# Performance work log

Measured on AMD Instinct MI355X. Metric: run time of the kernel, lower is better.

Reference implementation:

```python
import jax, jax.numpy as jnp
import numpy as np

H = 56; W = 56; WS = 7; SS = 3; HEADS = 12; DIM = 384

def _rel_pos_index(ws):
    coords = np.stack(np.meshgrid(np.arange(ws), np.arange(ws), indexing='ij'))  # (2, ws, ws)
    cf = coords.reshape(2, -1)
    rel = (cf[:, :, None] - cf[:, None, :]).transpose(1, 2, 0).astype(np.int64)  # (N, N, 2)
    rel[:, :, 0] += ws - 1
    rel[:, :, 1] += ws - 1
    rel[:, :, 0] *= 2 * ws - 1
    return jnp.asarray(rel.sum(-1))  # (N, N)

def _attn_mask(h, w, ws, ss):
    img = np.zeros((h, w))
    cnt = 0
    for hs in (slice(0, -ws), slice(-ws, -ss), slice(-ss, None)):
        for wsl in (slice(0, -ws), slice(-ws, -ss), slice(-ss, None)):
            img[hs, wsl] = cnt
            cnt += 1
    mw = img.reshape(h // ws, ws, w // ws, ws).transpose(0, 2, 1, 3).reshape(-1, ws * ws)
    am = mw[:, None, :] - mw[:, :, None]
    return jnp.asarray(np.where(am != 0, -100.0, 0.0).astype(np.float32))  # (nW, N, N)

REL_IDX = _rel_pos_index(WS)
ATTN_MASK = _attn_mask(H, W, WS, SS)

def _ln(x, g, b):
    mu = x.mean(-1, keepdims=True)
    var = x.var(-1, keepdims=True)  # biased, matches torch LayerNorm
    return (x - mu) / jnp.sqrt(var + 1e-5) * g + b

def setup_inputs():
    key = jax.random.key(0)
    ks = jax.random.split(key, 8)
    C = DIM
    Hd = 4 * C
    s = lambda k, shp: jax.random.normal(k, shp, jnp.float32) * 0.02
    return dict(
        x=jax.random.normal(ks[0], (32, H * W, C), jnp.float32),
        norm1_g=jnp.ones((C,), jnp.float32), norm1_b=jnp.zeros((C,), jnp.float32),
        qkv_w=s(ks[1], (3 * C, C)), qkv_b=jnp.zeros((3 * C,), jnp.float32),
        rpb_table=s(ks[2], ((2 * WS - 1) ** 2, HEADS)),
        proj_w=s(ks[3], (C, C)), proj_b=jnp.zeros((C,), jnp.float32),
        norm2_g=jnp.ones((C,), jnp.float32), norm2_b=jnp.zeros((C,), jnp.float32),
        fc1_w=s(ks[4], (Hd, C)), fc1_b=jnp.zeros((Hd,), jnp.float32),
        fc2_w=s(ks[5], (C, Hd)), fc2_b=jnp.zeros((C,), jnp.float32),
    )

def reference(x, norm1_g, norm1_b, qkv_w, qkv_b, rpb_table, proj_w, proj_b,
              norm2_g, norm2_b, fc1_w, fc1_b, fc2_w, fc2_b):
    B, L, C = x.shape
    h = HEADS
    d = C // h
    N = WS * WS
    nW = (H // WS) * (W // WS)
    shortcut = x
    y = _ln(x, norm1_g, norm1_b).reshape(B, H, W, C)
    # cyclic shift
    y = jnp.roll(y, (-SS, -SS), axis=(1, 2))
    # window partition -> (B*nW, N, C)
    y = y.reshape(B, H // WS, WS, W // WS, WS, C).transpose(0, 1, 3, 2, 4, 5).reshape(B * nW, N, C)
    # windowed attention
    qkv = (y @ qkv_w.T + qkv_b).reshape(B * nW, N, 3, h, d).transpose(2, 0, 3, 1, 4)
    q, k, v = qkv[0], qkv[1], qkv[2]  # (B*nW, h, N, d)
    scale = d ** -0.5
    attn = jnp.einsum('whnd,whmd->whnm', q * scale, k)
    bias = rpb_table[REL_IDX.reshape(-1)].reshape(N, N, h).transpose(2, 0, 1)  # (h, N, N)
    attn = attn + bias[None]
    attn = attn.reshape(B, nW, h, N, N) + ATTN_MASK[None, :, None]
    attn = jax.nn.softmax(attn.reshape(B * nW, h, N, N), axis=-1)
    out = jnp.einsum('whnm,whmd->whnd', attn, v).transpose(0, 2, 1, 3).reshape(B * nW, N, C)
    out = out @ proj_w.T + proj_b
    # window reverse -> (B, H, W, C)
    out = out.reshape(B, H // WS, W // WS, WS, WS, C).transpose(0, 1, 3, 2, 4, 5).reshape(B, H, W, C)
    # reverse cyclic shift
    out = jnp.roll(out, (SS, SS), axis=(1, 2)).reshape(B, L, C)
    x = shortcut + out
    m = _ln(x, norm2_g, norm2_b)
    m = jax.nn.gelu(m @ fc1_w.T + fc1_b, approximate=False) @ fc2_w.T + fc2_b
    return x + m
```

## Files before the change

### kernel.cpp

```cpp
#include <hip/hip_runtime.h>
#include <cstdint>
#include <cstddef>

typedef __bf16 bf16;
typedef __bf16 bf16x8 __attribute__((ext_vector_type(8)));
typedef float f32x4 __attribute__((ext_vector_type(4)));
typedef unsigned int u32;

__device__ __forceinline__ u32 pk(float a, float b) {
    u32 ua = __builtin_bit_cast(unsigned short, (bf16)a);
    u32 ub = __builtin_bit_cast(unsigned short, (bf16)b);
    return (ub << 16) | ua;
}

__device__ __forceinline__ void gld16(void* l, const void* g) {
    __builtin_amdgcn_global_load_lds(
        (const __attribute__((address_space(1))) void*)(size_t)g,
        (__attribute__((address_space(3))) void*)l, 16, 0, 0);
}

__global__ __launch_bounds__(256) void k_cvtw(
    const float* __restrict__ w0, const float* __restrict__ w1,
    const float* __restrict__ w2, const float* __restrict__ w3,
    bf16* __restrict__ o)
{
    int i = blockIdx.x * 256 + threadIdx.x;
    float v;
    if (i < 442368)       v = w0[i];
    else if (i < 589824)  v = w1[i - 442368];
    else if (i < 1179648) v = w2[i - 589824];
    else                  v = w3[i - 1179648];
    o[i] = (bf16)v;
}

__global__ __launch_bounds__(256) void k_bias(
    const float* __restrict__ rpb, float* __restrict__ ft)
{
    int t = blockIdx.x;
    int type = t / 12, head = t - (t / 12) * 12;
    for (int e = threadIdx.x; e < 4096; e += 256) {
        int i = e >> 6, j = e & 63;
        float v;
        if (j >= 49) v = -1e30f;
        else if (i >= 49) v = 0.f;
        else {
            int ri = i / 7, ci = i - ri * 7, rj = j / 7, cj = j - rj * 7;
            v = rpb[((ri - rj + 6) * 13 + (ci - cj + 6)) * 12 + head] * 1.4426950408889634f;
            int li = 0, lj = 0;
            if (type & 2) { li += (ri < 4) ? 3 : 6; lj += (rj < 4) ? 3 : 6; }
            if (type & 1) { li += (ci < 4) ? 1 : 2; lj += (cj < 4) ? 1 : 2; }
            if (li != lj) v -= 144.26950408889634f;
        }
        ft[(size_t)t * 4096 + e] = v;
    }
}

__global__ __launch_bounds__(256) void k_ln1(
    const float* __restrict__ x, const float* __restrict__ g,
    const float* __restrict__ b, bf16* __restrict__ ywin)
{
    int wv = threadIdx.x >> 6, lane = threadIdx.x & 63;
    int tok = blockIdx.x * 4 + wv;
    const float2* xp = (const float2*)(x + (size_t)tok * 384);
    float2 v[3];
    float s = 0.f, ss = 0.f;
    #pragma unroll
    for (int j = 0; j < 3; ++j) {
        v[j] = xp[j * 64 + lane];
        s += v[j].x + v[j].y; ss += v[j].x * v[j].x + v[j].y * v[j].y;
    }
    #pragma unroll
    for (int o = 32; o; o >>= 1) { s += __shfl_xor(s, o); ss += __shfl_xor(ss, o); }
    float mean = s * (1.f / 384.f);
    float rstd = rsqrtf(ss * (1.f / 384.f) - mean * mean + 1e-5f);
    int bi = tok / 3136, l = tok - bi * 3136;
    int h = l / 56, w = l - h * 56;
    int hs = h + 53; if (hs >= 56) hs -= 56;
    int ws = w + 53; if (ws >= 56) ws -= 56;
    int m = (bi * 64 + (hs / 7) * 8 + (ws / 7)) * 49 + (hs % 7) * 7 + (ws % 7);
    u32* op = (u32*)(ywin + (size_t)m * 384);
    const float2* g2 = (const float2*)g;
    const float2* b2 = (const float2*)b;
    #pragma unroll
    for (int j = 0; j < 3; ++j) {
        int c2 = j * 64 + lane;
        float2 gg = g2[c2], bb = b2[c2];
        op[c2] = pk((v[j].x - mean) * rstd * gg.x + bb.x,
                    (v[j].y - mean) * rstd * gg.y + bb.y);
    }
}

__global__ __launch_bounds__(256) void k_ln2(
    const float* __restrict__ x, const float* __restrict__ g,
    const float* __restrict__ b, bf16* __restrict__ y)
{
    int wv = threadIdx.x >> 6, lane = threadIdx.x & 63;
    int tok = blockIdx.x * 4 + wv;
    const float2* xp = (const float2*)(x + (size_t)tok * 384);
    float2 v[3];
    float s = 0.f, ss = 0.f;
    #pragma unroll
    for (int j = 0; j < 3; ++j) {
        v[j] = xp[j * 64 + lane];
        s += v[j].x + v[j].y; ss += v[j].x * v[j].x + v[j].y * v[j].y;
    }
    #pragma unroll
    for (int o = 32; o; o >>= 1) { s += __shfl_xor(s, o); ss += __shfl_xor(ss, o); }
    float mean = s * (1.f / 384.f);
    float rstd = rsqrtf(ss * (1.f / 384.f) - mean * mean + 1e-5f);
    u32* op = (u32*)(y + (size_t)tok * 384);
    const float2* g2 = (const float2*)g;
    const float2* b2 = (const float2*)b;
    #pragma unroll
    for (int j = 0; j < 3; ++j) {
        int c2 = j * 64 + lane;
        float2 gg = g2[c2], bb = b2[c2];
        op[c2] = pk((v[j].x - mean) * rstd * gg.x + bb.x,
                    (v[j].y - mean) * rstd * gg.y + bb.y);
    }
}

template<int EPI>
__global__ __launch_bounds__(256) void k_gemm(
    const bf16* __restrict__ A, const bf16* __restrict__ Bt,
    const float* __restrict__ bias, const float* __restrict__ resid,
    void* __restrict__ out, int N, int K, int nbn)
{
    __shared__ bf16 As[128 * 32];
    __shared__ bf16 Bs[128 * 32];

    int nwg = gridDim.x;
    int bid = blockIdx.x;
    int swz = (bid & 7) * (nwg >> 3) + (bid >> 3);
    int bm = swz / nbn, bn = swz % nbn;

    int tid  = threadIdx.x;
    int lane = tid & 63;
    int wv   = tid >> 6;
    int wr = wv >> 1, wc = wv & 1;
    int lr = lane & 15, lg = lane >> 4;

    int rowL = wv * 32 + (lane >> 2);
    int seg  = (lane & 3) ^ ((rowL >> 1) & 3);
    const bf16* ga0 = A  + (size_t)(bm * 128 + rowL) * K + seg * 8;
    const bf16* gb0 = Bt + (size_t)(bn * 128 + rowL) * K + seg * 8;
    const bf16* ga1 = ga0 + (size_t)16 * K;
    const bf16* gb1 = gb0 + (size_t)16 * K;
    bf16* lA0 = &As[(wv * 32) * 32];
    bf16* lA1 = &As[(wv * 32 + 16) * 32];
    bf16* lB0 = &Bs[(wv * 32) * 32];
    bf16* lB1 = &Bs[(wv * 32 + 16) * 32];

    f32x4 acc[4][4] = {};

    for (int k0 = 0; k0 < K; k0 += 32) {
        gld16(lA0, ga0 + k0); gld16(lA1, ga1 + k0);
        gld16(lB0, gb0 + k0); gld16(lB1, gb1 + k0);
        __syncthreads();
        bf16x8 af[4], bfr[4];
        #pragma unroll
        for (int i = 0; i < 4; ++i) {
            int ra = wr * 64 + i * 16 + lr;
            af[i]  = *(const bf16x8*)&As[ra * 32 + ((lg ^ ((ra >> 1) & 3)) << 3)];
            int rb = wc * 64 + i * 16 + lr;
            bfr[i] = *(const bf16x8*)&Bs[rb * 32 + ((lg ^ ((rb >> 1) & 3)) << 3)];
        }
        #pragma unroll
        for (int mi = 0; mi < 4; ++mi)
            #pragma unroll
            for (int ni = 0; ni < 4; ++ni)
                acc[mi][ni] = __builtin_amdgcn_mfma_f32_16x16x32_bf16(
                    af[mi], bfr[ni], acc[mi][ni], 0, 0, 0);
        __syncthreads();
    }

    int row0 = bm * 128 + wr * 64;
    int col0 = bn * 128 + wc * 64;
    #pragma unroll
    for (int mi = 0; mi < 4; ++mi)
    #pragma unroll
    for (int ni = 0; ni < 4; ++ni)
    #pragma unroll
    for (int r = 0; r < 4; ++r) {
        int gr = row0 + mi * 16 + lg * 4 + r;
        int gc = col0 + ni * 16 + lr;
        float v = acc[mi][ni][r] + bias[gc];
        if constexpr (EPI == 0) {
            if (gc < 384) v *= 0.25498226244716875f;
            ((bf16*)out)[(size_t)gr * N + gc] = (bf16)v;
        } else if constexpr (EPI == 1) {
            int bi = gr / 3136, rem = gr - bi * 3136;
            int win = rem / 49, pos = rem - win * 49;
            int hs = (win >> 3) * 7 + pos / 7;
            int ws = (win & 7) * 7 + pos % 7;
            hs += 3; if (hs >= 56) hs -= 56;
            ws += 3; if (ws >= 56) ws -= 56;
            size_t oi = ((size_t)bi * 3136 + hs * 56 + ws) * 384 + gc;
            ((float*)out)[oi] = resid[oi] + v;
        } else if constexpr (EPI == 2) {
            float ge = 0.5f * v * (1.f + erff(v * 0.70710678118654752f));
            ((bf16*)out)[(size_t)gr * N + gc] = (bf16)ge;
        } else {
            size_t oi = (size_t)gr * 384 + gc;
            ((float*)out)[oi] += v;
        }
    }
}

__global__ __launch_bounds__(256, 3) void k_attn(
    const bf16* __restrict__ qkv, const float* __restrict__ fusedT,
    bf16* __restrict__ outb)
{
    __shared__ bf16 vt[4][32 * 64];
    __shared__ bf16 pl[4][64 * 64];

    int bid = blockIdx.x;
    int swz = (bid & 7) * (6144 >> 3) + (bid >> 3);
    int window = swz / 3;
    int wv = threadIdx.x >> 6, lane = threadIdx.x & 63;
    int head = (swz - window * 3) * 4 + wv;
    int lr = lane & 15, lg = lane >> 4;

    size_t base = (size_t)window * 49 * 1152 + head * 32;
    const bf16* Qp = qkv + base;
    const bf16* Kp = qkv + base + 384;
    const bf16* Vp = qkv + base + 768;

    bf16* vts = vt[wv];
    #pragma unroll
    for (int t0 = 0; t0 < 8; ++t0) {
        int t = t0 * 64 + lane;
        int d = t >> 4, pos = 48 + (t & 15);
        vts[d * 64 + ((((pos >> 3) ^ (d & 7)) << 3) | (pos & 7))] = (bf16)0.f;
    }
    #pragma unroll
    for (int t0 = 0; t0 < 4; ++t0) {
        int t = t0 * 64 + lane;
        if (t < 196) {
            int pos = t >> 2, c8 = (t & 3) << 3;
            bf16x8 vv = *(const bf16x8*)(Vp + (size_t)pos * 1152 + c8);
            #pragma unroll
            for (int u = 0; u < 8; ++u) {
                int d = c8 + u;
                vts[d * 64 + ((((pos >> 3) ^ (d & 7)) << 3) | (pos & 7))] = vv[u];
            }
        }
    }

    bf16x8 kf[4], qf[4];
    #pragma unroll
    for (int t = 0; t < 4; ++t) {
        int row = t * 16 + lr; row = row > 48 ? 48 : row;
        kf[t] = *(const bf16x8*)(Kp + (size_t)row * 1152 + lg * 8);
        qf[t] = *(const bf16x8*)(Qp + (size_t)row * 1152 + lg * 8);
    }
    f32x4 st[4][4];
    #pragma unroll
    for (int a = 0; a < 4; ++a)
        #pragma unroll
        for (int c = 0; c < 4; ++c) st[a][c] = f32x4{0.f, 0.f, 0.f, 0.f};
    #pragma unroll
    for (int mj = 0; mj < 4; ++mj)
        #pragma unroll
        for (int ni = 0; ni < 4; ++ni)
            st[mj][ni] = __builtin_amdgcn_mfma_f32_16x16x32_bf16(
                kf[mj], qf[ni], st[mj][ni], 0, 0, 0);

    int wtype = (((window & 63) >= 56) ? 2 : 0) | (((window & 7) == 7) ? 1 : 0);
    const float* bt = fusedT + ((size_t)(wtype * 12 + head) << 12);
    #pragma unroll
    for (int ni = 0; ni < 4; ++ni)
        #pragma unroll
        for (int mj = 0; mj < 4; ++mj) {
            f32x4 bv = *(const f32x4*)(bt + (ni * 16 + lr) * 64 + mj * 16 + lg * 4);
            st[mj][ni] += bv;
        }

    #pragma unroll
    for (int ni = 0; ni < 4; ++ni) {
        float mx = -1e30f;
        #pragma unroll
        for (int mj = 0; mj < 4; ++mj)
            mx = fmaxf(mx, fmaxf(fmaxf(st[mj][ni][0], st[mj][ni][1]),
                                 fmaxf(st[mj][ni][2], st[mj][ni][3])));
        mx = fmaxf(mx, __shfl_xor(mx, 16));
        mx = fmaxf(mx, __shfl_xor(mx, 32));
        float l = 0.f;
        #pragma unroll
        for (int mj = 0; mj < 4; ++mj)
            #pragma unroll
            for (int r = 0; r < 4; ++r) {
                float p = exp2f(st[mj][ni][r] - mx);
                st[mj][ni][r] = p; l += p;
            }
        l += __shfl_xor(l, 16);
        l += __shfl_xor(l, 32);
        float rl = 1.f / l;
        #pragma unroll
        for (int mj = 0; mj < 4; ++mj)
            #pragma unroll
            for (int r = 0; r < 4; ++r) st[mj][ni][r] *= rl;
    }

    bf16* plw = pl[wv];
    #pragma unroll
    for (int mj = 0; mj < 4; ++mj)
        #pragma unroll
        for (int ni = 0; ni < 4; ++ni)
            #pragma unroll
            for (int hh = 0; hh < 2; ++hh) {
                u32 w = pk(st[mj][ni][hh * 2], st[mj][ni][hh * 2 + 1]);
                int j = mj * 16 + lg * 4 + hh * 2;
                int i = ni * 16 + lr;
                *(u32*)&plw[i * 64 + (((j >> 3) ^ (lr & 7)) << 3) + (j & 7)] = w;
            }

    bf16x8 pa[4][2], vf[2][2];
    #pragma unroll
    for (int mi = 0; mi < 4; ++mi)
        #pragma unroll
        for (int kk = 0; kk < 2; ++kk)
            pa[mi][kk] = *(const bf16x8*)&plw[(mi * 16 + lr) * 64 +
                                              (((kk * 4 + lg) ^ (lr & 7)) << 3)];
    #pragma unroll
    for (int td = 0; td < 2; ++td)
        #pragma unroll
        for (int kk = 0; kk < 2; ++kk)
            vf[td][kk] = *(const bf16x8*)&vts[(td * 16 + lr) * 64 +
                                              (((kk * 4 + lg) ^ (lr & 7)) << 3)];

    f32x4 o[4][2];
    #pragma unroll
    for (int a = 0; a < 4; ++a) { o[a][0] = f32x4{0.f,0.f,0.f,0.f}; o[a][1] = f32x4{0.f,0.f,0.f,0.f}; }
    #pragma unroll
    for (int kk = 0; kk < 2; ++kk)
        #pragma unroll
        for (int mi = 0; mi < 4; ++mi)
            #pragma unroll
            for (int td = 0; td < 2; ++td)
                o[mi][td] = __builtin_amdgcn_mfma_f32_16x16x32_bf16(
                    pa[mi][kk], vf[td][kk], o[mi][td], 0, 0, 0);

    bf16* op = outb + (size_t)window * 49 * 384 + head * 32;
    #pragma unroll
    for (int mi = 0; mi < 4; ++mi)
        #pragma unroll
        for (int r = 0; r < 4; ++r) {
            int i = mi * 16 + lg * 4 + r;
            if (i < 49) {
                #pragma unroll
                for (int td = 0; td < 2; ++td)
                    op[(size_t)i * 384 + td * 16 + lr] = (bf16)o[mi][td][r];
            }
        }
}

extern "C" void kernel_launch(void* const* d_in, const int* in_sizes, int n_in,
                              void* d_out, int out_size, void* d_ws, size_t ws_size,
                              hipStream_t stream)
{
    const float* x     = (const float*)d_in[0];
    const float* n1g   = (const float*)d_in[1];
    const float* n1b   = (const float*)d_in[2];
    const float* qkvw  = (const float*)d_in[3];
    const float* qkvb  = (const float*)d_in[4];
    const float* rpb   = (const float*)d_in[5];
    const float* projw = (const float*)d_in[6];
    const float* projb = (const float*)d_in[7];
    const float* n2g   = (const float*)d_in[8];
    const float* n2b   = (const float*)d_in[9];
    const float* fc1w  = (const float*)d_in[10];
    const float* fc1b  = (const float*)d_in[11];
    const float* fc2w  = (const float*)d_in[12];
    const float* fc2b  = (const float*)d_in[13];
    float* out = (float*)d_out;

    char* ws = (char*)d_ws;
    bf16* Wq   = (bf16*)(ws);
    bf16* Wp   = (bf16*)(ws + 884736);
    bf16* W1   = (bf16*)(ws + 1179648);
    bf16* W2   = (bf16*)(ws + 2359296);
    bf16* ywin = (bf16*)(ws + 3538944);
    bf16* qkv  = (bf16*)(ws + 80609280);
    bf16* attn = (bf16*)(ws + 311820288);
    bf16* hbuf = (bf16*)(ws + 80609280);
    bf16* y2   = ywin;
    float* fusedT = (float*)ws;

    k_cvtw<<<6912, 256, 0, stream>>>(qkvw, projw, fc1w, fc2w, Wq);
    k_ln1<<<25088, 256, 0, stream>>>(x, n1g, n1b, ywin);
    k_gemm<0><<<784 * 9, 256, 0, stream>>>(ywin, Wq, qkvb, nullptr, qkv, 1152, 384, 9);
    k_bias<<<48, 256, 0, stream>>>(rpb, fusedT);
    k_attn<<<6144, 256, 0, stream>>>(qkv, fusedT, attn);
    k_gemm<1><<<784 * 3, 256, 0, stream>>>(attn, Wp, projb, x, out, 384, 384, 3);
    k_ln2<<<25088, 256, 0, stream>>>(out, n2g, n2b, y2);
    k_gemm<2><<<784 * 12, 256, 0, stream>>>(y2, W1, fc1b, nullptr, hbuf, 1536, 384, 12);
    k_gemm<3><<<784 * 3, 256, 0, stream>>>(hbuf, W2, fc2b, nullptr, out, 384, 1536, 3);
}
```

Measured before the change: 1.229 ms.

## Triple-buffer GEMM LDS tiles with async global-to-LDS prefetch pipeline

Turns the GEMM main loop from a single-buffered load/sync/compute cycle into a 3-stage ring buffer in shared memory. The tile two steps ahead is issued with global_load_lds and explicit vmcnt waits, so memory latency overlaps MFMA work. It also raises wave priority around the MFMA block, hoists bias loads out of the epilogue, and sets launch_bounds to 2 blocks per SM. The cost is three times the LDS per block and hand-managed waitcnt logic, which depends on the per-thread load count staying at four.

```diff
diff --git a/kernel.cpp b/kernel.cpp
--- a/kernel.cpp
+++ b/kernel.cpp
@@ -121,13 +121,13 @@
 }
 
 template<int EPI>
-__global__ __launch_bounds__(256) void k_gemm(
+__global__ __launch_bounds__(256, 2) void k_gemm(
     const bf16* __restrict__ A, const bf16* __restrict__ Bt,
     const float* __restrict__ bias, const float* __restrict__ resid,
     void* __restrict__ out, int N, int K, int nbn)
 {
-    __shared__ bf16 As[128 * 32];
-    __shared__ bf16 Bs[128 * 32];
+    __shared__ bf16 As[3][128 * 32];
+    __shared__ bf16 Bs[3][128 * 32];
 
     int nwg = gridDim.x;
     int bid = blockIdx.x;
@@ -146,36 +146,69 @@
     const bf16* gb0 = Bt + (size_t)(bn * 128 + rowL) * K + seg * 8;
     const bf16* ga1 = ga0 + (size_t)16 * K;
     const bf16* gb1 = gb0 + (size_t)16 * K;
-    bf16* lA0 = &As[(wv * 32) * 32];
-    bf16* lA1 = &As[(wv * 32 + 16) * 32];
-    bf16* lB0 = &Bs[(wv * 32) * 32];
-    bf16* lB1 = &Bs[(wv * 32 + 16) * 32];
+    int lbase = wv * 32 * 32;
+
+    int col0 = bn * 128 + wc * 64;
+    float bv[4];
+    #pragma unroll
+    for (int ni = 0; ni < 4; ++ni) bv[ni] = bias[col0 + ni * 16 + lr];
 
     f32x4 acc[4][4] = {};
 
-    for (int k0 = 0; k0 < K; k0 += 32) {
-        gld16(lA0, ga0 + k0); gld16(lA1, ga1 + k0);
-        gld16(lB0, gb0 + k0); gld16(lB1, gb1 + k0);
-        __syncthreads();
+    auto STAGE = [&](int b, int k0) {
+        gld16(&As[b][lbase],           ga0 + k0);
+        gld16(&As[b][lbase + 16 * 32], ga1 + k0);
+        gld16(&Bs[b][lbase],           gb0 + k0);
+        gld16(&Bs[b][lbase + 16 * 32], gb1 + k0);
+    };
+    auto COMPUTE = [&](int b) {
+        const bf16* cA = As[b];
+        const bf16* cB = Bs[b];
         bf16x8 af[4], bfr[4];
         #pragma unroll
         for (int i = 0; i < 4; ++i) {
             int ra = wr * 64 + i * 16 + lr;
-            af[i]  = *(const bf16x8*)&As[ra * 32 + ((lg ^ ((ra >> 1) & 3)) << 3)];
+            af[i]  = *(const bf16x8*)&cA[ra * 32 + ((lg ^ ((ra >> 1) & 3)) << 3)];
             int rb = wc * 64 + i * 16 + lr;
-            bfr[i] = *(const bf16x8*)&Bs[rb * 32 + ((lg ^ ((rb >> 1) & 3)) << 3)];
-        }
+            bfr[i] = *(const bf16x8*)&cB[rb * 32 + ((lg ^ ((rb >> 1) & 3)) << 3)];
+        }
+        __builtin_amdgcn_s_setprio(1);
         #pragma unroll
         for (int mi = 0; mi < 4; ++mi)
             #pragma unroll
             for (int ni = 0; ni < 4; ++ni)
                 acc[mi][ni] = __builtin_amdgcn_mfma_f32_16x16x32_bf16(
                     af[mi], bfr[ni], acc[mi][ni], 0, 0, 0);
-        __syncthreads();
-    }
+        __builtin_amdgcn_s_setprio(0);
+    };
+
+    STAGE(0, 0);
+    STAGE(1, 32);
+    int cur = 0;
+    int k0 = 0;
+    for (; k0 + 64 < K; k0 += 32) {
+        int nb = cur + 2; if (nb >= 3) nb -= 3;
+        STAGE(nb, k0 + 64);
+        __builtin_amdgcn_sched_barrier(0);
+        asm volatile("s_waitcnt vmcnt(8)" ::: "memory");
+        __builtin_amdgcn_sched_barrier(0);
+        __builtin_amdgcn_s_barrier();
+        COMPUTE(cur);
+        __builtin_amdgcn_s_barrier();
+        cur = (cur + 1 == 3) ? 0 : cur + 1;
+    }
+    asm volatile("s_waitcnt vmcnt(4)" ::: "memory");
+    __builtin_amdgcn_sched_barrier(0);
+    __builtin_amdgcn_s_barrier();
+    COMPUTE(cur);
+    __builtin_amdgcn_s_barrier();
+    cur = (cur + 1 == 3) ? 0 : cur + 1;
+    asm volatile("s_waitcnt vmcnt(0)" ::: "memory");
+    __builtin_amdgcn_sched_barrier(0);
+    __builtin_amdgcn_s_barrier();
+    COMPUTE(cur);
 
     int row0 = bm * 128 + wr * 64;
-    int col0 = bn * 128 + wc * 64;
     #pragma unroll
     for (int mi = 0; mi < 4; ++mi)
     #pragma unroll
@@ -184,7 +217,7 @@
     for (int r = 0; r < 4; ++r) {
         int gr = row0 + mi * 16 + lg * 4 + r;
         int gc = col0 + ni * 16 + lr;
-        float v = acc[mi][ni][r] + bias[gc];
+        float v = acc[mi][ni][r] + bv[ni];
         if constexpr (EPI == 0) {
             if (gc < 384) v *= 0.25498226244716875f;
             ((bf16*)out)[(size_t)gr * N + gc] = (bf16)v;
```

Measured after the change: 1.129 ms. 1.09x faster.
